# Kernel tuning notes

Measured on AMD Instinct MI355X. Metric: run time of the kernel, lower is better.

Reference implementation:

```python
import jax, jax.numpy as jnp
import numpy as np
from functools import partial

N_FIXED, B, L, T, K = 64, 5000, 10, 25, 8
N = 1_000_000


def setup_inputs() -> dict:
    key = jax.random.key(0)
    ks = jax.random.split(key, 8)
    X = jax.random.normal(ks[0], (N, N_FIXED), dtype=jnp.float32)
    batter_ids = jax.random.randint(ks[1], (N,), 0, B)
    league_ids = jax.random.randint(ks[2], (N,), 0, L)
    season_ids = jax.random.randint(ks[3], (N,), 0, T)
    # learned parameters (match torch init: beta=0, raw_rho=0 -> use small noise
    # for a non-degenerate reference; Sigma = identity per head K)
    beta = jax.random.normal(ks[4], (N_FIXED, K), dtype=jnp.float32) * 0.02
    raw_rho = jax.random.normal(ks[5], (L, K), dtype=jnp.float32) * 0.1
    Sigma = jnp.tile(jnp.eye(L, dtype=jnp.float32)[None], (K, 1, 1))
    eps = jax.random.normal(ks[6], (B, L, T, K), dtype=jnp.float32)
    return {"X": X, "batter_ids": batter_ids, "league_ids": league_ids,
            "season_ids": season_ids, "beta": beta, "raw_rho": raw_rho,
            "Sigma": Sigma, "eps": eps}


def _random_effects(raw_rho, Sigma, eps):
    # SigmaHalf: (K,L,L); torch einsum 'KLL,BLK->BLK' repeats L -> diagonal only
    SigmaHalf = jnp.linalg.cholesky(Sigma)
    d = jnp.diagonal(SigmaHalf, axis1=1, axis2=2).T      # (L,K)
    rho = jnp.tanh(raw_rho)                              # (L,K)
    e = jnp.transpose(eps, (2, 0, 1, 3))                 # (T,B,L,K)
    u0 = e[0]                                            # u_0 = eps_0 (no scaling)

    def step(u_prev, eps_t):
        u = rho * u_prev + d * eps_t
        return u, u

    _, us = jax.lax.scan(step, u0, e[1:])                # (T-1,B,L,K)
    return jnp.concatenate([u0[None], us], axis=0)       # (T,B,L,K)


def reference(X, batter_ids, league_ids, season_ids, beta, raw_rho, Sigma, eps):
    fixed = X @ beta                                     # (n,K)
    u = _random_effects(raw_rho, Sigma, eps)             # (T,B,L,K)
    rand = u[season_ids, batter_ids, league_ids, :]      # (n,K) gather
    return fixed + rand
```

## Files before the change

kernel.cpp:

```cpp
#include <hip/hip_runtime.h>
#include <math.h>

#define NROWS 1000000
#define NF    64
#define BB    5000
#define LLg   10
#define TTg   25
#define KKg   8

#define WS_RHO   0
#define WS_D     80
#define WS_BETAT 160
#define WS_U     1024

__global__ void prep_kernel(const float* __restrict__ beta,
                            const float* __restrict__ raw_rho,
                            const float* __restrict__ Sigma,
                            float* __restrict__ ws) {
    const int tid = threadIdx.x;
    for (int i = tid; i < LLg * KKg; i += blockDim.x)
        ws[WS_RHO + i] = tanhf(raw_rho[i]);
    for (int i = tid; i < KKg * NF; i += blockDim.x) {
        const int k = i / NF, f = i % NF;
        ws[WS_BETAT + i] = beta[f * KKg + k];
    }
    if (tid < KKg) {
        const int k = tid;
        float Lf[LLg][LLg];
        const float* S = Sigma + k * LLg * LLg;
        for (int i = 0; i < LLg; ++i) {
            for (int j = 0; j <= i; ++j) {
                float s = S[i * LLg + j];
                for (int m = 0; m < j; ++m) s -= Lf[i][m] * Lf[j][m];
                if (i == j) Lf[i][i] = sqrtf(s);
                else        Lf[i][j] = s / Lf[j][j];
            }
        }
        for (int l = 0; l < LLg; ++l)
            ws[WS_D + l * KKg + k] = Lf[l][l];
    }
}

__global__ __launch_bounds__(256) void u_kernel(const float* __restrict__ eps,
                                                const float* __restrict__ ws,
                                                float* __restrict__ u) {
    const int tid = blockIdx.x * blockDim.x + threadIdx.x;
    if (tid >= BB * LLg * KKg) return;
    const int k = tid % KKg;
    const int l = (tid / KKg) % LLg;
    const int b = tid / (KKg * LLg);
    const float rho = ws[WS_RHO + l * KKg + k];
    const float dv  = ws[WS_D   + l * KKg + k];
    const float* ep = eps + ((size_t)(b * LLg + l) * TTg) * KKg + k;
    float* up = u + (size_t)(b * LLg + l) * KKg + k;
    const size_t ustride = (size_t)BB * LLg * KKg;
    float uv = ep[0];
    up[0] = uv;
    for (int t = 1; t < TTg; ++t) {
        uv = rho * uv + dv * ep[(size_t)t * KKg];
        up[(size_t)t * ustride] = uv;
    }
}

template <bool USE_TABLE>
__global__ __launch_bounds__(256) void main_kernel(
    const float* __restrict__ X,
    const int*   __restrict__ bat,
    const int*   __restrict__ lea,
    const int*   __restrict__ sea,
    const float* __restrict__ ws,
    const float* __restrict__ u_table,
    const float* __restrict__ eps,
    float*       __restrict__ out)
{
    const int gt  = blockIdx.x * blockDim.x + threadIdx.x;
    const int c   = gt & 7;
    const int g   = gt >> 3;
    const int row0 = g * 2;

    const int b0 = bat[row0],     b1 = bat[row0 + 1];
    const int l0 = lea[row0],     l1 = lea[row0 + 1];
    const int t0 = sea[row0],     t1 = sea[row0 + 1];

    float uv0, uv1;
    if (USE_TABLE) {
        uv0 = u_table[(((size_t)t0 * BB + b0) * LLg + l0) * KKg + c];
        uv1 = u_table[(((size_t)t1 * BB + b1) * LLg + l1) * KKg + c];
    } else {
        const float rho0 = ws[WS_RHO + l0 * KKg + c];
        const float dv0  = ws[WS_D   + l0 * KKg + c];
        const float* e0  = eps + ((size_t)(b0 * LLg + l0) * TTg) * KKg + c;
        uv0 = e0[0];
        for (int tt = 1; tt <= t0; ++tt) uv0 = rho0 * uv0 + dv0 * e0[(size_t)tt * KKg];
        const float rho1 = ws[WS_RHO + l1 * KKg + c];
        const float dv1  = ws[WS_D   + l1 * KKg + c];
        const float* e1  = eps + ((size_t)(b1 * LLg + l1) * TTg) * KKg + c;
        uv1 = e1[0];
        for (int tt = 1; tt <= t1; ++tt) uv1 = rho1 * uv1 + dv1 * e1[(size_t)tt * KKg];
    }

    float bc[NF];
    const float4* bt4 = (const float4*)(ws + WS_BETAT + c * NF);
#pragma unroll
    for (int j = 0; j < NF / 4; ++j) {
        const float4 v = bt4[j];
        bc[4 * j + 0] = v.x; bc[4 * j + 1] = v.y;
        bc[4 * j + 2] = v.z; bc[4 * j + 3] = v.w;
    }

    const float4* x4 = (const float4*)(X + (size_t)row0 * NF);
    float acc0 = 0.f, acc1 = 0.f;
#pragma unroll
    for (int j = 0; j < NF / 4; ++j) {
        const float4 v = x4[j];
        acc0 += v.x * bc[4 * j + 0] + v.y * bc[4 * j + 1]
              + v.z * bc[4 * j + 2] + v.w * bc[4 * j + 3];
    }
#pragma unroll
    for (int j = 0; j < NF / 4; ++j) {
        const float4 v = x4[NF / 4 + j];
        acc1 += v.x * bc[4 * j + 0] + v.y * bc[4 * j + 1]
              + v.z * bc[4 * j + 2] + v.w * bc[4 * j + 3];
    }

    out[(size_t)row0 * KKg + c]       = acc0 + uv0;
    out[(size_t)(row0 + 1) * KKg + c] = acc1 + uv1;
}

extern "C" void kernel_launch(void* const* d_in, const int* in_sizes, int n_in,
                              void* d_out, int out_size, void* d_ws, size_t ws_size,
                              hipStream_t stream) {
    const float* X       = (const float*)d_in[0];
    const int*   bat     = (const int*)  d_in[1];
    const int*   lea     = (const int*)  d_in[2];
    const int*   sea     = (const int*)  d_in[3];
    const float* beta    = (const float*)d_in[4];
    const float* raw_rho = (const float*)d_in[5];
    const float* Sigma   = (const float*)d_in[6];
    const float* eps     = (const float*)d_in[7];
    float* out = (float*)d_out;
    float* ws  = (float*)d_ws;
    float* u   = ws + WS_U;

    const size_t need_bytes = ((size_t)WS_U + (size_t)TTg * BB * LLg * KKg) * sizeof(float);
    const bool use_table = ws_size >= need_bytes;

    prep_kernel<<<1, 256, 0, stream>>>(beta, raw_rho, Sigma, ws);

    const int nthreads = (NROWS / 2) * KKg;
    const int nblocks  = nthreads / 256;

    if (use_table) {
        u_kernel<<<(BB * LLg * KKg + 255) / 256, 256, 0, stream>>>(eps, ws, u);
        main_kernel<true><<<nblocks, 256, 0, stream>>>(X, bat, lea, sea, ws, u, eps, out);
    } else {
        main_kernel<false><<<nblocks, 256, 0, stream>>>(X, bat, lea, sea, ws, u, eps, out);
    }
}
```

Before: 496.3 us.

## Split X row across 8 lanes with shuffle-reduce and shared-memory beta

```diff
diff --git a/kernel.cpp b/kernel.cpp
--- a/kernel.cpp
+++ b/kernel.cpp
@@ -10,20 +10,14 @@
 
 #define WS_RHO   0
 #define WS_D     80
-#define WS_BETAT 160
 #define WS_U     1024
 
-__global__ void prep_kernel(const float* __restrict__ beta,
-                            const float* __restrict__ raw_rho,
+__global__ void prep_kernel(const float* __restrict__ raw_rho,
                             const float* __restrict__ Sigma,
                             float* __restrict__ ws) {
     const int tid = threadIdx.x;
     for (int i = tid; i < LLg * KKg; i += blockDim.x)
         ws[WS_RHO + i] = tanhf(raw_rho[i]);
-    for (int i = tid; i < KKg * NF; i += blockDim.x) {
-        const int k = i / NF, f = i % NF;
-        ws[WS_BETAT + i] = beta[f * KKg + k];
-    }
     if (tid < KKg) {
         const int k = tid;
         float Lf[LLg][LLg];
@@ -68,63 +62,103 @@
     const int*   __restrict__ bat,
     const int*   __restrict__ lea,
     const int*   __restrict__ sea,
+    const float* __restrict__ beta,
     const float* __restrict__ ws,
     const float* __restrict__ u_table,
     const float* __restrict__ eps,
     float*       __restrict__ out)
 {
-    const int gt  = blockIdx.x * blockDim.x + threadIdx.x;
-    const int c   = gt & 7;
-    const int g   = gt >> 3;
+    __shared__ float sbeta[8 * 68];
+    for (int i = threadIdx.x; i < NF * KKg; i += blockDim.x) {
+        const int f = i >> 3, k = i & 7;
+        sbeta[(f >> 3) * 68 + (f & 7) * 8 + k] = beta[i];
+    }
+    __syncthreads();
+
+    const int gt   = blockIdx.x * blockDim.x + threadIdx.x;
+    const int j    = gt & 7;
+    const int g    = gt >> 3;
     const int row0 = g * 2;
 
-    const int b0 = bat[row0],     b1 = bat[row0 + 1];
-    const int l0 = lea[row0],     l1 = lea[row0 + 1];
-    const int t0 = sea[row0],     t1 = sea[row0 + 1];
+    const int2 bb = *(const int2*)(bat + row0);
+    const int2 ll = *(const int2*)(lea + row0);
+    const int2 tt = *(const int2*)(sea + row0);
+
+    const float* xr0p = X + (size_t)row0 * NF + j * 8;
+    const float* xr1p = X + (size_t)(row0 + 1) * NF + j * 8;
+    float xr0[8], xr1[8];
+    *(float4*)&xr0[0] = ((const float4*)xr0p)[0];
+    *(float4*)&xr0[4] = ((const float4*)xr0p)[1];
+    *(float4*)&xr1[0] = ((const float4*)xr1p)[0];
+    *(float4*)&xr1[4] = ((const float4*)xr1p)[1];
 
     float uv0, uv1;
     if (USE_TABLE) {
-        uv0 = u_table[(((size_t)t0 * BB + b0) * LLg + l0) * KKg + c];
-        uv1 = u_table[(((size_t)t1 * BB + b1) * LLg + l1) * KKg + c];
+        uv0 = u_table[(((size_t)tt.x * BB + bb.x) * LLg + ll.x) * KKg + j];
+        uv1 = u_table[(((size_t)tt.y * BB + bb.y) * LLg + ll.y) * KKg + j];
     } else {
-        const float rho0 = ws[WS_RHO + l0 * KKg + c];
-        const float dv0  = ws[WS_D   + l0 * KKg + c];
-        const float* e0  = eps + ((size_t)(b0 * LLg + l0) * TTg) * KKg + c;
+        const float rho0 = ws[WS_RHO + ll.x * KKg + j];
+        const float dv0  = ws[WS_D   + ll.x * KKg + j];
+        const float* e0  = eps + ((size_t)(bb.x * LLg + ll.x) * TTg) * KKg + j;
         uv0 = e0[0];
-        for (int tt = 1; tt <= t0; ++tt) uv0 = rho0 * uv0 + dv0 * e0[(size_t)tt * KKg];
-        const float rho1 = ws[WS_RHO + l1 * KKg + c];
-        const float dv1  = ws[WS_D   + l1 * KKg + c];
-        const float* e1  = eps + ((size_t)(b1 * LLg + l1) * TTg) * KKg + c;
+        for (int s = 1; s <= tt.x; ++s) uv0 = rho0 * uv0 + dv0 * e0[(size_t)s * KKg];
+        const float rho1 = ws[WS_RHO + ll.y * KKg + j];
+        const float dv1  = ws[WS_D   + ll.y * KKg + j];
+        const float* e1  = eps + ((size_t)(bb.y * LLg + ll.y) * TTg) * KKg + j;
         uv1 = e1[0];
-        for (int tt = 1; tt <= t1; ++tt) uv1 = rho1 * uv1 + dv1 * e1[(size_t)tt * KKg];
+        for (int s = 1; s <= tt.y; ++s) uv1 = rho1 * uv1 + dv1 * e1[(size_t)s * KKg];
     }
 
-    float bc[NF];
-    const float4* bt4 = (const float4*)(ws + WS_BETAT + c * NF);
+    float bv[8][8];
 #pragma unroll
-    for (int j = 0; j < NF / 4; ++j) {
-        const float4 v = bt4[j];
-        bc[4 * j + 0] = v.x; bc[4 * j + 1] = v.y;
-        bc[4 * j + 2] = v.z; bc[4 * j + 3] = v.w;
+    for (int ff = 0; ff < 8; ++ff) {
+        const float4* p = (const float4*)&sbeta[j * 68 + ff * 8];
+        const float4 u0 = p[0], u1 = p[1];
+        bv[ff][0] = u0.x; bv[ff][1] = u0.y; bv[ff][2] = u0.z; bv[ff][3] = u0.w;
+        bv[ff][4] = u1.x; bv[ff][5] = u1.y; bv[ff][6] = u1.z; bv[ff][7] = u1.w;
     }
 
-    const float4* x4 = (const float4*)(X + (size_t)row0 * NF);
-    float acc0 = 0.f, acc1 = 0.f;
+    float p0[8], p1[8];
 #pragma unroll
-    for (int j = 0; j < NF / 4; ++j) {
-        const float4 v = x4[j];
-        acc0 += v.x * bc[4 * j + 0] + v.y * bc[4 * j + 1]
-              + v.z * bc[4 * j + 2] + v.w * bc[4 * j + 3];
+    for (int k = 0; k < 8; ++k) { p0[k] = 0.f; p1[k] = 0.f; }
+#pragma unroll
+    for (int ff = 0; ff < 8; ++ff) {
+#pragma unroll
+        for (int k = 0; k < 8; ++k) {
+            p0[k] += xr0[ff] * bv[ff][k];
+            p1[k] += xr1[ff] * bv[ff][k];
+        }
+    }
+
+#pragma unroll
+    for (int i = 0; i < 4; ++i) {
+        const float s0 = (j & 4) ? p0[i] : p0[i + 4];
+        const float s1 = (j & 4) ? p1[i] : p1[i + 4];
+        const float k0 = (j & 4) ? p0[i + 4] : p0[i];
+        const float k1 = (j & 4) ? p1[i + 4] : p1[i];
+        p0[i] = k0 + __shfl_xor(s0, 4);
+        p1[i] = k1 + __shfl_xor(s1, 4);
     }
 #pragma unroll
-    for (int j = 0; j < NF / 4; ++j) {
-        const float4 v = x4[NF / 4 + j];
-        acc1 += v.x * bc[4 * j + 0] + v.y * bc[4 * j + 1]
-              + v.z * bc[4 * j + 2] + v.w * bc[4 * j + 3];
+    for (int i = 0; i < 2; ++i) {
+        const float s0 = (j & 2) ? p0[i] : p0[i + 2];
+        const float s1 = (j & 2) ? p1[i] : p1[i + 2];
+        const float k0 = (j & 2) ? p0[i + 2] : p0[i];
+        const float k1 = (j & 2) ? p1[i + 2] : p1[i];
+        p0[i] = k0 + __shfl_xor(s0, 2);
+        p1[i] = k1 + __shfl_xor(s1, 2);
+    }
+    {
+        const float s0 = (j & 1) ? p0[0] : p0[1];
+        const float s1 = (j & 1) ? p1[0] : p1[1];
+        const float k0 = (j & 1) ? p0[1] : p0[0];
+        const float k1 = (j & 1) ? p1[1] : p1[0];
+        p0[0] = k0 + __shfl_xor(s0, 1);
+        p1[0] = k1 + __shfl_xor(s1, 1);
     }
 
-    out[(size_t)row0 * KKg + c]       = acc0 + uv0;
-    out[(size_t)(row0 + 1) * KKg + c] = acc1 + uv1;
+    out[(size_t)row0 * KKg + j]       = p0[0] + uv0;
+    out[(size_t)(row0 + 1) * KKg + j] = p1[0] + uv1;
 }
 
 extern "C" void kernel_launch(void* const* d_in, const int* in_sizes, int n_in,
@@ -145,15 +179,15 @@
     const size_t need_bytes = ((size_t)WS_U + (size_t)TTg * BB * LLg * KKg) * sizeof(float);
     const bool use_table = ws_size >= need_bytes;
 
-    prep_kernel<<<1, 256, 0, stream>>>(beta, raw_rho, Sigma, ws);
+    prep_kernel<<<1, 128, 0, stream>>>(raw_rho, Sigma, ws);
 
     const int nthreads = (NROWS / 2) * KKg;
     const int nblocks  = nthreads / 256;
 
     if (use_table) {
         u_kernel<<<(BB * LLg * KKg + 255) / 256, 256, 0, stream>>>(eps, ws, u);
-        main_kernel<true><<<nblocks, 256, 0, stream>>>(X, bat, lea, sea, ws, u, eps, out);
+        main_kernel<true><<<nblocks, 256, 0, stream>>>(X, bat, lea, sea, beta, ws, u, eps, out);
     } else {
-        main_kernel<false><<<nblocks, 256, 0, stream>>>(X, bat, lea, sea, ws, u, eps, out);
+        main_kernel<false><<<nblocks, 256, 0, stream>>>(X, bat, lea, sea, beta, ws, u, eps, out);
     }
 }
```

New measurement: 400.6 us. 1.24x faster.
